# Performance work log

Measured on AMD Instinct MI355X. Metric: run time of the kernel, lower is better.

The kernel has to match this reference:

```python
import jax, jax.numpy as jnp
import numpy as np

B, LV, LT, D, TD, H = 64, 1024, 128, 256, 1536, 4
HD = D // H
KEEP_RATIO = 0.5
K = min(max(int(np.ceil(LV * KEEP_RATIO)), 1), LV)
ND = LV - K  # number of dropped tokens
EPS_NORM = 1e-12


def setup_inputs() -> dict:
    key = jax.random.key(0)
    ks = jax.random.split(key, 9)
    s = 0.02
    return {
        "hidden_v": jax.random.normal(ks[0], (B, LV, D), jnp.float32),
        "hidden_t": jax.random.normal(ks[1], (B, LT, TD), jnp.float32),
        "senti_t": jax.random.normal(ks[2], (B, LT), jnp.float32),
        "mask_v": jnp.ones((B, LV), dtype=bool),
        "mask_t": jnp.ones((B, LT), dtype=bool),
        "W_t": jax.random.normal(ks[3], (D, TD), jnp.float32) * s,
        "b_t": jnp.zeros((D,), jnp.float32),
        "Wq": jax.random.normal(ks[4], (D, D), jnp.float32) * s,
        "bq": jnp.zeros((D,), jnp.float32),
        "Wk": jax.random.normal(ks[5], (D, D), jnp.float32) * s,
        "bk": jnp.zeros((D,), jnp.float32),
    }


def _l2norm(x):
    n = jnp.linalg.norm(x, axis=-1, keepdims=True)
    return x / jnp.maximum(n, EPS_NORM)


def _prune_one(V_b, score_b):
    """V_b: [LV, D], score_b: [LV] -> (V_merge [K, D], top_idx [K])."""
    _, top_idx = jax.lax.top_k(score_b, K)
    top_idx = jnp.sort(top_idx)
    V_keep = V_b[top_idx]                       # [K, D]
    drop_mask = jnp.ones((LV,), bool).at[top_idx].set(False)
    ar = jnp.arange(LV)
    drop_idx = jnp.sort(jnp.where(drop_mask, ar, LV + ar))[:ND]  # [ND], sorted
    V_drop = V_b[drop_idx]                      # [ND, D]
    score_drop = score_b[drop_idx]              # [ND]
    # bipartite cosine-similarity assignment of dropped -> kept
    sim = _l2norm(V_drop) @ _l2norm(V_keep).T   # [ND, K]
    assign = jnp.argmax(sim, axis=1)            # [ND]
    # per-cluster softmax over dropped-token scores (segment softmax)
    seg_max = jax.ops.segment_max(score_drop, assign, num_segments=K)
    w = jnp.exp(score_drop - seg_max[assign])
    denom = jax.ops.segment_sum(w, assign, num_segments=K)
    w = w / jnp.maximum(denom[assign], EPS_NORM)
    merged = jax.ops.segment_sum(w[:, None] * V_drop, assign, num_segments=K)
    has_member = jax.ops.segment_sum(jnp.ones((ND,), V_b.dtype), assign, num_segments=K) > 0
    V_merge = _l2norm(V_keep + merged)
    V_out = jnp.where(has_member[:, None], V_merge, V_keep)
    return V_out, top_idx


def reference(hidden_v, hidden_t, senti_t, mask_v, mask_t, W_t, b_t, Wq, bq, Wk, bk):
    mt = mask_t.astype(jnp.float32)
    # text projection + sentiment weights
    T = hidden_t @ W_t.T + b_t                                   # [B, LT, D]
    w_t = jnp.abs(senti_t) * mt
    w_t = w_t / (w_t.sum(axis=1, keepdims=True) + 1e-8)
    w_t = w_t * mt
    # cross-attention weights (averaged over heads); attn_out is unused by the module
    q = (hidden_v @ Wq.T + bq).reshape(B, LV, H, HD)
    k = (T @ Wk.T + bk).reshape(B, LT, H, HD)
    scores = jnp.einsum('bqhd,bkhd->bhqk', q, k) / np.sqrt(HD)   # [B, H, LV, LT]
    scores = jnp.where(mask_t[:, None, None, :], scores, -1e9)
    attn = jax.nn.softmax(scores, axis=-1).mean(axis=1)          # [B, LV, LT]
    score_v = jnp.einsum('bqk,bk->bq', attn, w_t)                # [B, LV]
    score_v = jnp.where(mask_v, score_v, -1e9)
    hidden_v_new, retained_indices = jax.vmap(_prune_one)(hidden_v, score_v)
    return hidden_v_new, retained_indices
```

## Files before the change

### kernel.cpp

```cpp
#include <hip/hip_runtime.h>
#include <math.h>

#define B_ 64
#define LV_ 1024
#define LT_ 128
#define D_ 256
#define TD_ 1536
#define H_ 4
#define HD_ 64
#define K_ 512
#define ND_ 512

__device__ float g_M[TD_ * D_];
__device__ float g_WqT[D_ * D_];
__device__ float g_WkT[D_ * D_];
__device__ float g_kbias[D_];
__device__ float g_wt[B_ * LT_];
__device__ float g_Kmat[(size_t)B_ * LT_ * D_];
__device__ float g_score[B_ * LV_];
__device__ int   g_tidx[B_ * K_];
__device__ int   g_didx[B_ * ND_];
__device__ float g_sdrop[B_ * ND_];
__device__ int   g_assign[B_ * ND_];
__device__ float g_kninv[B_ * K_];


__device__ __forceinline__ float f4c(const float4& v, int i) {
  return ((const float*)&v)[i];
}

__global__ __launch_bounds__(256) void prep1_kernel(
    const float* __restrict__ Wk, const float* __restrict__ Wq,
    const float* __restrict__ bt, const float* __restrict__ bk) {
  int bx = blockIdx.x, t = threadIdx.x;
  if (bx < D_) {
    g_WkT[bx * D_ + t] = Wk[t * D_ + bx];
  } else if (bx < 2 * D_) {
    int j = bx - D_;
    g_WqT[j * D_ + t] = Wq[t * D_ + j];
  } else {
    float acc = bk[t];
    for (int e = 0; e < D_; ++e) acc += bt[e] * Wk[t * D_ + e];
    g_kbias[t] = acc;
  }
}

__global__ __launch_bounds__(256) void prep2_kernel(const float* __restrict__ Wt) {
  int j0 = blockIdx.x * 16;
  int t = threadIdx.x;
  __shared__ float WtL[256 * 20];
  const float4* Wt4 = (const float4*)Wt;
#pragma unroll
  for (int i = 0; i < 4; ++i) {
    int idx = i * 256 + t;
    int e = idx >> 2, j4 = idx & 3;
    float4 v = Wt4[e * (TD_ / 4) + (j0 >> 2) + j4];
    WtL[e * 20 + 4 * j4 + 0] = v.x;
    WtL[e * 20 + 4 * j4 + 1] = v.y;
    WtL[e * 20 + 4 * j4 + 2] = v.z;
    WtL[e * 20 + 4 * j4 + 3] = v.w;
  }
  __syncthreads();
  float acc[16];
#pragma unroll
  for (int jj = 0; jj < 16; ++jj) acc[jj] = 0.f;
  for (int e = 0; e < D_; ++e) {
    float wk = g_WkT[e * D_ + t];
#pragma unroll
    for (int q4 = 0; q4 < 4; ++q4) {
      float4 w = *(const float4*)&WtL[e * 20 + 4 * q4];
      acc[4 * q4 + 0] += w.x * wk;
      acc[4 * q4 + 1] += w.y * wk;
      acc[4 * q4 + 2] += w.z * wk;
      acc[4 * q4 + 3] += w.w * wk;
    }
  }
#pragma unroll
  for (int jj = 0; jj < 16; ++jj) g_M[(j0 + jj) * D_ + t] = acc[jj];
}

__global__ __launch_bounds__(128) void wt_kernel(const float* __restrict__ senti) {
  int b = blockIdx.x, t = threadIdx.x;
  __shared__ float red[128];
  float v = fabsf(senti[b * LT_ + t]);
  red[t] = v;
  __syncthreads();
  for (int s = 64; s > 0; s >>= 1) {
    if (t < s) red[t] += red[t + s];
    __syncthreads();
  }
  g_wt[b * LT_ + t] = v / (red[0] + 1e-8f);
}

__global__ __launch_bounds__(256) void kproj_kernel(const float* __restrict__ ht) {
  int b = blockIdx.x >> 3;
  int l0 = (blockIdx.x & 7) * 16;
  int t = threadIdx.x;
  __shared__ float htT[256 * 20];
  int lq = t >> 6;
  int dq = t & 63;
  float acc[4][4];
#pragma unroll
  for (int li = 0; li < 4; ++li)
#pragma unroll
    for (int di = 0; di < 4; ++di) acc[li][di] = 0.f;
  const float4* M4 = (const float4*)g_M;
  const float4* ht4 = (const float4*)ht;
  for (int e0 = 0; e0 < TD_; e0 += 256) {
    __syncthreads();
#pragma unroll
    for (int i = 0; i < 4; ++i) {
      int idx = i * 256 + t;
      int e4 = idx >> 4, l = idx & 15;
      float4 v = ht4[(size_t)(b * LT_ + l0 + l) * (TD_ / 4) + (e0 >> 2) + e4];
      htT[(4 * e4 + 0) * 20 + l] = v.x;
      htT[(4 * e4 + 1) * 20 + l] = v.y;
      htT[(4 * e4 + 2) * 20 + l] = v.z;
      htT[(4 * e4 + 3) * 20 + l] = v.w;
    }
    __syncthreads();
    for (int e = 0; e < 256; ++e) {
      float4 m = M4[(size_t)(e0 + e) * 64 + dq];
      float4 hl = *(const float4*)&htT[e * 20 + 4 * lq];
#pragma unroll
      for (int li = 0; li < 4; ++li) {
        float hs = f4c(hl, li);
        acc[li][0] += hs * m.x;
        acc[li][1] += hs * m.y;
        acc[li][2] += hs * m.z;
        acc[li][3] += hs * m.w;
      }
    }
  }
  float4 kb = *(const float4*)(g_kbias + 4 * dq);
#pragma unroll
  for (int li = 0; li < 4; ++li) {
    float4 o = make_float4(acc[li][0] + kb.x, acc[li][1] + kb.y,
                           acc[li][2] + kb.z, acc[li][3] + kb.w);
    ((float4*)g_Kmat)[(size_t)(b * LT_ + l0 + 4 * lq + li) * 64 + dq] = o;
  }
}

__global__ __launch_bounds__(256, 3) void score_kernel(
    const float* __restrict__ hv, const float* __restrict__ bq) {
  int b = blockIdx.y;
  int q0 = blockIdx.x * 32;
  int t = threadIdx.x;
  __shared__ float qR[32 * 256];
  __shared__ float kT[32 * 128];
  int co = t & 31;
  int rq = t >> 5;
  {
    float acc[4][8];
#pragma unroll
    for (int c = 0; c < 8; ++c) {
      float bqv = bq[8 * co + c];
#pragma unroll
      for (int ri = 0; ri < 4; ++ri) acc[ri][c] = bqv;
    }
    const float4* hv4 = (const float4*)(hv + ((size_t)b * LV_ + q0) * D_);
    for (int j4 = 0; j4 < 64; ++j4) {
      float4 hq[4];
#pragma unroll
      for (int ri = 0; ri < 4; ++ri) hq[ri] = hv4[(4 * rq + ri) * 64 + j4];
#pragma unroll
      for (int jj = 0; jj < 4; ++jj) {
        const float4* w4 = (const float4*)(g_WqT + (4 * j4 + jj) * D_ + 8 * co);
        float4 wa = w4[0], wb = w4[1];
#pragma unroll
        for (int ri = 0; ri < 4; ++ri) {
          float hvv = f4c(hq[ri], jj);
          acc[ri][0] += hvv * wa.x;
          acc[ri][1] += hvv * wa.y;
          acc[ri][2] += hvv * wa.z;
          acc[ri][3] += hvv * wa.w;
          acc[ri][4] += hvv * wb.x;
          acc[ri][5] += hvv * wb.y;
          acc[ri][6] += hvv * wb.z;
          acc[ri][7] += hvv * wb.w;
        }
      }
    }
    float4* qR4w = (float4*)qR;
#pragma unroll
    for (int ri = 0; ri < 4; ++ri) {
      qR4w[(4 * rq + ri) * 64 + 2 * co + 0] =
          make_float4(acc[ri][0], acc[ri][1], acc[ri][2], acc[ri][3]);
      qR4w[(4 * rq + ri) * 64 + 2 * co + 1] =
          make_float4(acc[ri][4], acc[ri][5], acc[ri][6], acc[ri][7]);
    }
  }
  int qq = rq;
  int kq = co;
  float4 wtv = ((const float4*)(g_wt + b * LT_))[kq];
  float svacc[4] = {0.f, 0.f, 0.f, 0.f};
  const float4* km4 = ((const float4*)g_Kmat) + (size_t)b * LT_ * 64;
  const float4* qR4 = (const float4*)qR;
  const float4* kT4 = (const float4*)kT;
  for (int h = 0; h < H_; ++h) {
    float sacc[4][4];
#pragma unroll
    for (int ri = 0; ri < 4; ++ri)
#pragma unroll
      for (int ki = 0; ki < 4; ++ki) sacc[ri][ki] = 0.f;
    for (int half = 0; half < 2; ++half) {
      __syncthreads();
      {
#pragma unroll
        for (int i = 0; i < 4; ++i) {
          int idx = i * 256 + t;
          int k = idx >> 3, d4 = idx & 7;
          float4 v = km4[k * 64 + h * 16 + half * 8 + d4];
          int ksw = ((((k >> 2) ^ d4) << 2) | (k & 3));
          kT[(4 * d4 + 0) * 128 + ksw] = v.x;
          kT[(4 * d4 + 1) * 128 + ksw] = v.y;
          kT[(4 * d4 + 2) * 128 + ksw] = v.z;
          kT[(4 * d4 + 3) * 128 + ksw] = v.w;
        }
      }
      __syncthreads();
#pragma unroll
      for (int d4l = 0; d4l < 8; ++d4l) {
        float4 qv[4], kv[4];
#pragma unroll
        for (int ri = 0; ri < 4; ++ri)
          qv[ri] = qR4[(4 * qq + ri) * 64 + h * 16 + half * 8 + d4l];
#pragma unroll
        for (int dd = 0; dd < 4; ++dd)
          kv[dd] = kT4[(4 * d4l + dd) * 32 + (kq ^ d4l)];
#pragma unroll
        for (int dd = 0; dd < 4; ++dd)
#pragma unroll
          for (int ri = 0; ri < 4; ++ri) {
            float qs = f4c(qv[ri], dd);
            sacc[ri][0] += qs * kv[dd].x;
            sacc[ri][1] += qs * kv[dd].y;
            sacc[ri][2] += qs * kv[dd].z;
            sacc[ri][3] += qs * kv[dd].w;
          }
      }
    }
#pragma unroll
    for (int ri = 0; ri < 4; ++ri) {
      float s0 = sacc[ri][0] * 0.125f, s1 = sacc[ri][1] * 0.125f;
      float s2 = sacc[ri][2] * 0.125f, s3 = sacc[ri][3] * 0.125f;
      float m = fmaxf(fmaxf(s0, s1), fmaxf(s2, s3));
#pragma unroll
      for (int off = 16; off > 0; off >>= 1) m = fmaxf(m, __shfl_xor(m, off));
      float e0 = expf(s0 - m), e1 = expf(s1 - m);
      float e2 = expf(s2 - m), e3 = expf(s3 - m);
      float es = e0 + e1 + e2 + e3;
      float cs = e0 * wtv.x + e1 * wtv.y + e2 * wtv.z + e3 * wtv.w;
#pragma unroll
      for (int off = 16; off > 0; off >>= 1) {
        es += __shfl_xor(es, off);
        cs += __shfl_xor(cs, off);
      }
      svacc[ri] += cs / es;
    }
  }
  if (kq == 0) {
#pragma unroll
    for (int ri = 0; ri < 4; ++ri)
      g_score[(size_t)b * LV_ + q0 + 4 * qq + ri] = svacc[ri] * 0.25f;
  }
}

__global__ __launch_bounds__(1024) void topk_kernel(float* __restrict__ out_idx) {
  int b = blockIdx.x, t = threadIdx.x;
  __shared__ float s[LV_];
  __shared__ unsigned char keep[LV_];
  s[t] = g_score[(size_t)b * LV_ + t];
  __syncthreads();
  float mys = s[t];
  int cnt = 0;
  for (int jj = 0; jj < LV_; ++jj) {
    float sj = s[jj];
    cnt += (sj > mys || (sj == mys && jj < t)) ? 1 : 0;
  }
  int kp = (cnt < K_) ? 1 : 0;
  keep[t] = (unsigned char)kp;
  __syncthreads();
  int pos = 0;
  for (int jj = 0; jj < t; ++jj) pos += keep[jj];
  if (kp) {
    g_tidx[b * K_ + pos] = t;
    out_idx[b * K_ + pos] = (float)t;
  } else {
    int dp = t - pos;
    g_didx[b * ND_ + dp] = t;
    g_sdrop[b * ND_ + dp] = mys;
  }
}

__global__ __launch_bounds__(256) void knorm_kernel(const float* __restrict__ hv) {
  int b = blockIdx.y;
  int k = blockIdx.x * 256 + threadIdx.x;
  int src = g_tidx[b * K_ + k];
  const float4* row = (const float4*)(hv + ((size_t)b * LV_ + src) * D_);
  float acc = 0.f;
  for (int c = 0; c < 64; ++c) {
    float4 v = row[c];
    acc += v.x * v.x;
    acc += v.y * v.y;
    acc += v.z * v.z;
    acc += v.w * v.w;
  }
  g_kninv[b * K_ + k] = 1.f / fmaxf(sqrtf(acc), 1e-12f);
}

__global__ __launch_bounds__(256, 3) void assign_kernel(const float* __restrict__ hv) {
  int b = blockIdx.y;
  int n0 = blockIdx.x * 32;
  int t = threadIdx.x;
  __shared__ float smem[32 * 9 * 4 + 32 * 128];
  float* VdL = smem;
  float* VkT = smem + 1152;
  float* bestv = smem;
  int* bestk = (int*)(smem + 1024);

  int tn = t >> 5;
  int tk = t & 31;
  int rstage = t >> 3;
  int c8 = t & 7;

  int didx_t = g_didx[b * ND_ + n0 + rstage];
  const float4* vd_src = (const float4*)(hv + ((size_t)b * LV_ + didx_t) * D_);

  float bv[4] = {-INFINITY, -INFINITY, -INFINITY, -INFINITY};
  int bk[4] = {0, 0, 0, 0};

  for (int kt = 0; kt < 4; ++kt) {
    const float4* vk_src[4];
#pragma unroll
    for (int i = 0; i < 4; ++i) {
      int kl = i * 32 + rstage;
      int tix = g_tidx[b * K_ + kt * 128 + kl];
      vk_src[i] = (const float4*)(hv + ((size_t)b * LV_ + tix) * D_);
    }
    float4 kn4 = ((const float4*)(g_kninv + (size_t)b * K_ + kt * 128))[tk];
    float acc[4][4][4];
#pragma unroll
    for (int ri = 0; ri < 4; ++ri)
#pragma unroll
      for (int kj = 0; kj < 4; ++kj)
#pragma unroll
        for (int c = 0; c < 4; ++c) acc[ri][kj][c] = 0.f;
    for (int dc = 0; dc < 8; ++dc) {
      __syncthreads();
      {
        float4 v = vd_src[dc * 8 + c8];
        ((float4*)VdL)[rstage * 9 + c8] = v;
      }
#pragma unroll
      for (int i = 0; i < 4; ++i) {
        int kl = i * 32 + rstage;
        float4 v = vk_src[i][dc * 8 + c8];
        int col = ((((kl >> 2) ^ c8) << 2) | (kl & 3));
        VkT[(4 * c8 + 0) * 128 + col] = v.x;
        VkT[(4 * c8 + 1) * 128 + col] = v.y;
        VkT[(4 * c8 + 2) * 128 + col] = v.z;
        VkT[(4 * c8 + 3) * 128 + col] = v.w;
      }
      __syncthreads();
      const float4* VdL4 = (const float4*)VdL;
      const float4* VkT4 = (const float4*)VkT;
#pragma unroll
      for (int d4l = 0; d4l < 8; ++d4l) {
        float4 vd[4], kv[4];
#pragma unroll
        for (int ri = 0; ri < 4; ++ri)
          vd[ri] = VdL4[(4 * tn + ri) * 9 + d4l];
#pragma unroll
        for (int dd = 0; dd < 4; ++dd)
          kv[dd] = VkT4[(4 * d4l + dd) * 32 + (tk ^ d4l)];
#pragma unroll
        for (int dd = 0; dd < 4; ++dd)
#pragma unroll
          for (int ri = 0; ri < 4; ++ri) {
            float a = f4c(vd[ri], dd);
            acc[ri][0][dd] += a * kv[dd].x;
            acc[ri][1][dd] += a * kv[dd].y;
            acc[ri][2][dd] += a * kv[dd].z;
            acc[ri][3][dd] += a * kv[dd].w;
          }
      }
    }
#pragma unroll
    for (int ri = 0; ri < 4; ++ri) {
#pragma unroll
      for (int kj = 0; kj < 4; ++kj) {
        float s = (acc[ri][kj][0] + acc[ri][kj][1]) + (acc[ri][kj][2] + acc[ri][kj][3]);
        float v = s * f4c(kn4, kj);
        int kg = kt * 128 + 4 * tk + kj;
        if (v > bv[ri]) { bv[ri] = v; bk[ri] = kg; }
      }
    }
  }
  __syncthreads();
#pragma unroll
  for (int ri = 0; ri < 4; ++ri) {
    bestv[(4 * tn + ri) * 32 + tk] = bv[ri];
    bestk[(4 * tn + ri) * 32 + tk] = bk[ri];
  }
  __syncthreads();
  if (t < 32) {
    float bvf = bestv[t * 32];
    int bkf = bestk[t * 32];
    for (int q = 1; q < 32; ++q) {
      float v = bestv[t * 32 + q];
      int kx = bestk[t * 32 + q];
      if (v > bvf || (v == bvf && kx < bkf)) { bvf = v; bkf = kx; }
    }
    g_assign[b * ND_ + n0 + t] = bkf;
  }
}

__global__ __launch_bounds__(64) void merge_kernel(
    const float* __restrict__ hv, float* __restrict__ out_v) {
  int b = blockIdx.y, k = blockIdx.x;
  int lane = threadIdx.x;
  __shared__ int mem[ND_];
  int base = 0;
  for (int c = 0; c < ND_; c += 64) {
    int a = g_assign[b * ND_ + c + lane];
    unsigned long long msk = __ballot(a == k);
    if (a == k) {
      int pos = base + __popcll(msk & ((1ULL << lane) - 1ULL));
      mem[pos] = c + lane;
    }
    base += __popcll(msk);
  }
  __syncthreads();
  int src = g_tidx[b * K_ + k];
  float4 vk = ((const float4*)(hv + ((size_t)b * LV_ + src) * D_))[lane];
  float4 res;
  if (base > 0) {
    float mx = -INFINITY;
    for (int i = lane; i < base; i += 64) mx = fmaxf(mx, g_sdrop[b * ND_ + mem[i]]);
#pragma unroll
    for (int o = 32; o > 0; o >>= 1) mx = fmaxf(mx, __shfl_xor(mx, o));
    float dsum = 0.f;
    for (int i = lane; i < base; i += 64) dsum += expf(g_sdrop[b * ND_ + mem[i]] - mx);
#pragma unroll
    for (int o = 32; o > 0; o >>= 1) dsum += __shfl_xor(dsum, o);
    dsum = fmaxf(dsum, 1e-12f);
    float4 acc = {0.f, 0.f, 0.f, 0.f};
    for (int i = 0; i < base; ++i) {
      int n = mem[i];
      float w = expf(g_sdrop[b * ND_ + n] - mx) / dsum;
      float4 ud = ((const float4*)(hv + ((size_t)b * LV_ + g_didx[b * ND_ + n]) * D_))[lane];
      acc.x += w * ud.x; acc.y += w * ud.y;
      acc.z += w * ud.z; acc.w += w * ud.w;
    }
    float4 s4 = {vk.x + acc.x, vk.y + acc.y, vk.z + acc.z, vk.w + acc.w};
    float ss = s4.x * s4.x + s4.y * s4.y + s4.z * s4.z + s4.w * s4.w;
#pragma unroll
    for (int o = 32; o > 0; o >>= 1) ss += __shfl_xor(ss, o);
    float scale = 1.f / fmaxf(sqrtf(ss), 1e-12f);
    res.x = s4.x * scale; res.y = s4.y * scale; res.z = s4.z * scale; res.w = s4.w * scale;
  } else {
    res = vk;
  }
  ((float4*)(out_v + ((size_t)b * K_ + k) * D_))[lane] = res;
}

extern "C" void kernel_launch(void* const* d_in, const int* in_sizes, int n_in,
                              void* d_out, int out_size, void* d_ws, size_t ws_size,
                              hipStream_t stream) {
  const float* hv = (const float*)d_in[0];
  const float* ht = (const float*)d_in[1];
  const float* senti = (const float*)d_in[2];
  const float* Wt = (const float*)d_in[5];
  const float* bt = (const float*)d_in[6];
  const float* Wq = (const float*)d_in[7];
  const float* bq = (const float*)d_in[8];
  const float* Wk = (const float*)d_in[9];
  const float* bk = (const float*)d_in[10];
  (void)in_sizes; (void)n_in; (void)out_size; (void)d_ws; (void)ws_size;

  float* out_v = (float*)d_out;
  float* out_idx = out_v + (size_t)B_ * K_ * D_;

  hipLaunchKernelGGL(prep1_kernel, dim3(2 * D_ + 1), dim3(256), 0, stream, Wk, Wq, bt, bk);
  hipLaunchKernelGGL(prep2_kernel, dim3(TD_ / 16), dim3(256), 0, stream, Wt);
  hipLaunchKernelGGL(wt_kernel, dim3(B_), dim3(128), 0, stream, senti);
  hipLaunchKernelGGL(kproj_kernel, dim3(B_ * 8), dim3(256), 0, stream, ht);
  hipLaunchKernelGGL(score_kernel, dim3(LV_ / 32, B_), dim3(256), 0, stream, hv, bq);
  hipLaunchKernelGGL(topk_kernel, dim3(B_), dim3(1024), 0, stream, out_idx);
  hipLaunchKernelGGL(knorm_kernel, dim3(2, B_), dim3(256), 0, stream, hv);
  hipLaunchKernelGGL(assign_kernel, dim3(ND_ / 32, B_), dim3(128 / 4 * 8), 0, stream, hv);
  hipLaunchKernelGGL(merge_kernel, dim3(K_, B_), dim3(64), 0, stream, hv, out_v);
}
```

Before: 796.3 us.

## Store projected keys transposed and read them directly in score kernel

The key projection kernel now stages its output tile through shared memory and writes K in a transposed [B, D, LT] layout. The score kernel then loads key vectors straight from global memory (coalesced float4 per lane) instead of copying them into a swizzled LDS tile each head-half. This removes per-head barriers and 16KB of LDS, so the occupancy hint rises from 3 to 5 blocks. The trade-off is that K reads now rely on L1/L2 caching instead of LDS, and kproj gains an extra shared-memory transpose step.

```diff
diff --git a/kernel.cpp b/kernel.cpp
--- a/kernel.cpp
+++ b/kernel.cpp
@@ -16,7 +16,7 @@
 __device__ float g_WkT[D_ * D_];
 __device__ float g_kbias[D_];
 __device__ float g_wt[B_ * LT_];
-__device__ float g_Kmat[(size_t)B_ * LT_ * D_];
+__device__ float g_KmatT[(size_t)B_ * D_ * LT_];
 __device__ float g_score[B_ * LV_];
 __device__ int   g_tidx[B_ * K_];
 __device__ int   g_didx[B_ * ND_];
@@ -133,21 +133,34 @@
     }
   }
   float4 kb = *(const float4*)(g_kbias + 4 * dq);
+  __syncthreads();
 #pragma unroll
   for (int li = 0; li < 4; ++li) {
-    float4 o = make_float4(acc[li][0] + kb.x, acc[li][1] + kb.y,
-                           acc[li][2] + kb.z, acc[li][3] + kb.w);
-    ((float4*)g_Kmat)[(size_t)(b * LT_ + l0 + 4 * lq + li) * 64 + dq] = o;
-  }
-}
-
-__global__ __launch_bounds__(256, 3) void score_kernel(
+    float o0 = acc[li][0] + kb.x;
+    float o1 = acc[li][1] + kb.y;
+    float o2 = acc[li][2] + kb.z;
+    float o3 = acc[li][3] + kb.w;
+    int l = 4 * lq + li;
+    htT[(4 * dq + 0) * 17 + l] = o0;
+    htT[(4 * dq + 1) * 17 + l] = o1;
+    htT[(4 * dq + 2) * 17 + l] = o2;
+    htT[(4 * dq + 3) * 17 + l] = o3;
+  }
+  __syncthreads();
+#pragma unroll
+  for (int i = 0; i < 16; ++i) {
+    int idx = i * 256 + t;
+    int l = idx & 15, d = idx >> 4;
+    g_KmatT[((size_t)b * D_ + d) * LT_ + l0 + l] = htT[d * 17 + l];
+  }
+}
+
+__global__ __launch_bounds__(256, 5) void score_kernel(
     const float* __restrict__ hv, const float* __restrict__ bq) {
   int b = blockIdx.y;
   int q0 = blockIdx.x * 32;
   int t = threadIdx.x;
   __shared__ float qR[32 * 256];
-  __shared__ float kT[32 * 128];
   int co = t & 31;
   int rq = t >> 5;
   {
@@ -190,55 +203,38 @@
           make_float4(acc[ri][4], acc[ri][5], acc[ri][6], acc[ri][7]);
     }
   }
+  __syncthreads();
   int qq = rq;
   int kq = co;
   float4 wtv = ((const float4*)(g_wt + b * LT_))[kq];
   float svacc[4] = {0.f, 0.f, 0.f, 0.f};
-  const float4* km4 = ((const float4*)g_Kmat) + (size_t)b * LT_ * 64;
+  const float4* kmt4 = (const float4*)(g_KmatT + (size_t)b * D_ * LT_);
   const float4* qR4 = (const float4*)qR;
-  const float4* kT4 = (const float4*)kT;
   for (int h = 0; h < H_; ++h) {
     float sacc[4][4];
 #pragma unroll
     for (int ri = 0; ri < 4; ++ri)
 #pragma unroll
       for (int ki = 0; ki < 4; ++ki) sacc[ri][ki] = 0.f;
-    for (int half = 0; half < 2; ++half) {
-      __syncthreads();
-      {
-#pragma unroll
-        for (int i = 0; i < 4; ++i) {
-          int idx = i * 256 + t;
-          int k = idx >> 3, d4 = idx & 7;
-          float4 v = km4[k * 64 + h * 16 + half * 8 + d4];
-          int ksw = ((((k >> 2) ^ d4) << 2) | (k & 3));
-          kT[(4 * d4 + 0) * 128 + ksw] = v.x;
-          kT[(4 * d4 + 1) * 128 + ksw] = v.y;
-          kT[(4 * d4 + 2) * 128 + ksw] = v.z;
-          kT[(4 * d4 + 3) * 128 + ksw] = v.w;
+#pragma unroll
+    for (int d4 = 0; d4 < 16; ++d4) {
+      float4 qv[4], kv[4];
+#pragma unroll
+      for (int ri = 0; ri < 4; ++ri)
+        qv[ri] = qR4[(4 * qq + ri) * 64 + h * 16 + d4];
+#pragma unroll
+      for (int dd = 0; dd < 4; ++dd)
+        kv[dd] = kmt4[(size_t)(h * 64 + 4 * d4 + dd) * 32 + kq];
+#pragma unroll
+      for (int dd = 0; dd < 4; ++dd)
+#pragma unroll
+        for (int ri = 0; ri < 4; ++ri) {
+          float qs = f4c(qv[ri], dd);
+          sacc[ri][0] += qs * kv[dd].x;
+          sacc[ri][1] += qs * kv[dd].y;
+          sacc[ri][2] += qs * kv[dd].z;
+          sacc[ri][3] += qs * kv[dd].w;
         }
-      }
-      __syncthreads();
-#pragma unroll
-      for (int d4l = 0; d4l < 8; ++d4l) {
-        float4 qv[4], kv[4];
-#pragma unroll
-        for (int ri = 0; ri < 4; ++ri)
-          qv[ri] = qR4[(4 * qq + ri) * 64 + h * 16 + half * 8 + d4l];
-#pragma unroll
-        for (int dd = 0; dd < 4; ++dd)
-          kv[dd] = kT4[(4 * d4l + dd) * 32 + (kq ^ d4l)];
-#pragma unroll
-        for (int dd = 0; dd < 4; ++dd)
-#pragma unroll
-          for (int ri = 0; ri < 4; ++ri) {
-            float qs = f4c(qv[ri], dd);
-            sacc[ri][0] += qs * kv[dd].x;
-            sacc[ri][1] += qs * kv[dd].y;
-            sacc[ri][2] += qs * kv[dd].z;
-            sacc[ri][3] += qs * kv[dd].w;
-          }
-      }
     }
 #pragma unroll
     for (int ri = 0; ri < 4; ++ri) {
@@ -489,6 +485,6 @@
   hipLaunchKernelGGL(score_kernel, dim3(LV_ / 32, B_), dim3(256), 0, stream, hv, bq);
   hipLaunchKernelGGL(topk_kernel, dim3(B_), dim3(1024), 0, stream, out_idx);
   hipLaunchKernelGGL(knorm_kernel, dim3(2, B_), dim3(256), 0, stream, hv);
-  hipLaunchKernelGGL(assign_kernel, dim3(ND_ / 32, B_), dim3(128 / 4 * 8), 0, stream, hv);
+  hipLaunchKernelGGL(assign_kernel, dim3(ND_ / 32, B_), dim3(256), 0, stream, hv);
   hipLaunchKernelGGL(merge_kernel, dim3(K_, B_), dim3(64), 0, stream, hv, out_v);
 }
```

New measurement: 834.3 us. +4.8%, slower.
